# Kernel tuning notes

Hardware: AMD Instinct MI355X
Metric: run time of the kernel (lower is better)

Reference implementation:

```python
import jax, jax.numpy as jnp
import numpy as np

P = 16  # patch size
D = 768  # embedding dim


def setup_inputs() -> dict:
    key = jax.random.key(0)
    k_img, k_w, k_b = jax.random.split(key, 3)
    B, H, W, C = 64, 224, 224, 3
    image = jax.random.normal(k_img, (B, H, W, C), dtype=jnp.float32)
    patch_dim = P * P * C  # 768
    # Keras Dense default: glorot_uniform kernel, zeros bias
    limit = np.sqrt(6.0 / (patch_dim + D)).astype(np.float32)
    W_proj = jax.random.uniform(k_w, (patch_dim, D), dtype=jnp.float32,
                                minval=-limit, maxval=limit)
    b_proj = jnp.zeros((D,), dtype=jnp.float32)
    return {"image": image, "W_proj": W_proj, "b_proj": b_proj}


def reference(image, W_proj, b_proj):
    B, H, W, C = image.shape
    nh, nw = H // P, W // P
    # Fused im2col replacing the per-patch slicing loop:
    # [B,H,W,C] -> [B, nh, P, nw, P, C] -> [B, nh, nw, P, P, C] -> [B, nh*nw, P*P*C]
    # Row-major (p_i, p_j) patch order matches the original nested loop, and
    # flatten of a [B,P,P,C] slice matches the (P,P,C) raveling here.
    patches = image.reshape(B, nh, P, nw, P, C)
    patches = patches.transpose(0, 1, 3, 2, 4, 5).reshape(B, nh * nw, P * P * C)
    # Dense + exact GELU (tf.keras.activations.gelu default approximate=False)
    x = jnp.einsum('bnp,pd->bnd', patches, W_proj) + b_proj
    return jax.nn.gelu(x, approximate=False)
```

## Files before the change

### kernel.cpp

```cpp
#include <hip/hip_runtime.h>
#include <hip/hip_bf16.h>
#include <math.h>

#define MM 12544
#define KK 768
#define NN 768
#define BM 64
#define BN 256
#define BK 64
#define KT 12
#define MT 196
#define NT 3
#define TILE_A_BYTES (BM*BK*2)
#define TILE_B_BYTES (BN*BK*2)

#define IM2COL_BLOCKS ((MM * 96) / 256)
#define WTPACK_BLOCKS ((NN * 96) / 256)

typedef __bf16 v8bf __attribute__((ext_vector_type(8)));
typedef float  v4f  __attribute__((ext_vector_type(4)));

__global__ __launch_bounds__(256) void pack_kernel(const float* __restrict__ img,
                                                   const float* __restrict__ w,
                                                   __hip_bfloat16* __restrict__ apack,
                                                   __hip_bfloat16* __restrict__ wpack) {
    if (blockIdx.x < IM2COL_BLOCKS) {
        int tid = blockIdx.x * 256 + threadIdx.x;
        int gg  = tid % 96;
        int m   = tid / 96;
        int b   = m / 196;
        int pm  = m - b * 196;
        int pr  = pm / 14;
        int pc  = pm - pr * 14;
        int k0  = gg * 8;
        int i   = k0 / 48;
        int rem = k0 - i * 48;
        const float* src = img + (size_t)(((b * 224 + pr * 16 + i) * 224 + pc * 16) * 3 + rem);
        float4 f0 = *(const float4*)src;
        float4 f1 = *(const float4*)(src + 4);
        int mt = m >> 6;
        int r  = m & 63;
        int kt = gg >> 3;
        int g  = gg & 7;
        int gs = g ^ (r & 7);
        union { __hip_bfloat16 h[8]; uint4 u; } o;
        o.h[0] = __float2bfloat16(f0.x); o.h[1] = __float2bfloat16(f0.y);
        o.h[2] = __float2bfloat16(f0.z); o.h[3] = __float2bfloat16(f0.w);
        o.h[4] = __float2bfloat16(f1.x); o.h[5] = __float2bfloat16(f1.y);
        o.h[6] = __float2bfloat16(f1.z); o.h[7] = __float2bfloat16(f1.w);
        *(uint4*)(apack + ((size_t)(mt * KT + kt) * BM + r) * BK + gs * 8) = o.u;
    } else {
        int tid = (blockIdx.x - IM2COL_BLOCKS) * 256 + threadIdx.x;
        int n   = tid % 768;
        int gg  = tid / 768;
        int k0  = gg * 8;
        float f[8];
#pragma unroll
        for (int j = 0; j < 8; j++) f[j] = w[(size_t)(k0 + j) * NN + n];
        int nt = n >> 8;
        int nr = n & 255;
        int kt = gg >> 3;
        int g  = gg & 7;
        int gs = g ^ (nr & 7);
        union { __hip_bfloat16 h[8]; uint4 u; } o;
#pragma unroll
        for (int j = 0; j < 8; j++) o.h[j] = __float2bfloat16(f[j]);
        *(uint4*)(wpack + ((size_t)(nt * KT + kt) * BN + nr) * BK + gs * 8) = o.u;
    }
}

__device__ __forceinline__ float gelu_fast(float x) {
    float t2 = 1.5957691216057308f * x * (1.0f + 0.044715f * x * x);
    float e  = __expf(t2);
    float r  = __builtin_amdgcn_rcpf(e + 1.0f);
    return x - x * r;
}

__global__ __launch_bounds__(256, 3) void gemm_gelu(const __hip_bfloat16* __restrict__ apack,
                                                    const __hip_bfloat16* __restrict__ wpack,
                                                    const float* __restrict__ bias,
                                                    float* __restrict__ out) {
    __shared__ __align__(16) __hip_bfloat16 As[BM * BK];
    __shared__ __align__(16) __hip_bfloat16 Bs[BN * BK];

    const int blk = blockIdx.x;
    const int nt  = blk % 3;
    const int mt  = blk / 3;

    const int tid  = threadIdx.x;
    const int lane = tid & 63;
    const int wave = tid >> 6;
    const int wn   = wave * 64;
    const int col  = lane & 15;
    const int quad = lane >> 4;
    const int cl7  = col & 7;

    v4f acc[4][4];
    const v4f vzero = {0.f, 0.f, 0.f, 0.f};
#pragma unroll
    for (int a = 0; a < 4; a++)
#pragma unroll
        for (int c = 0; c < 4; c++) acc[a][c] = vzero;

    const char* aT = (const char*)apack + (size_t)mt * KT * TILE_A_BYTES;
    const char* bT = (const char*)wpack + (size_t)nt * KT * TILE_B_BYTES;

    for (int kt = 0; kt < KT; kt++) {
#pragma unroll
        for (int p = 0; p < 2; p++) {
            int off = p * 4096 + tid * 16;
            __builtin_amdgcn_global_load_lds(
                (const __attribute__((address_space(1))) void*)(aT + off),
                (__attribute__((address_space(3))) void*)((char*)As + off), 16, 0, 0);
        }
#pragma unroll
        for (int p = 0; p < 8; p++) {
            int off = p * 4096 + tid * 16;
            __builtin_amdgcn_global_load_lds(
                (const __attribute__((address_space(1))) void*)(bT + off),
                (__attribute__((address_space(3))) void*)((char*)Bs + off), 16, 0, 0);
        }
        aT += TILE_A_BYTES;
        bT += TILE_B_BYTES;
        __syncthreads();

#pragma unroll
        for (int ks = 0; ks < 2; ks++) {
            const int gs = (ks * 4 + quad) ^ cl7;
            const v8bf* pa = (const v8bf*)(As + col * BK + gs * 8);
            const v8bf* pb = (const v8bf*)(Bs + (wn + col) * BK + gs * 8);
            v8bf af[4], bfr[4];
#pragma unroll
            for (int mi = 0; mi < 4; mi++) af[mi] = pa[mi * 128];
#pragma unroll
            for (int ni = 0; ni < 4; ni++) bfr[ni] = pb[ni * 128];
#pragma unroll
            for (int mi = 0; mi < 4; mi++)
#pragma unroll
                for (int ni = 0; ni < 4; ni++)
                    acc[mi][ni] = __builtin_amdgcn_mfma_f32_16x16x32_bf16(
                        af[mi], bfr[ni], acc[mi][ni], 0, 0, 0);
        }
        __syncthreads();
    }

#pragma unroll
    for (int ni = 0; ni < 4; ni++) {
        int n    = nt * BN + wn + ni * 16 + col;
        float bv = bias[n];
#pragma unroll
        for (int mi = 0; mi < 4; mi++) {
            int rowb = mt * BM + mi * 16 + quad * 4;
            float* po = out + (size_t)rowb * NN + n;
#pragma unroll
            for (int rg = 0; rg < 4; rg++) {
                float x = acc[mi][ni][rg] + bv;
                po[(size_t)rg * NN] = gelu_fast(x);
            }
        }
    }
}

extern "C" void kernel_launch(void* const* d_in, const int* in_sizes, int n_in,
                              void* d_out, int out_size, void* d_ws, size_t ws_size,
                              hipStream_t stream) {
    const float* img   = (const float*)d_in[0];
    const float* wproj = (const float*)d_in[1];
    const float* bias  = (const float*)d_in[2];
    float* out = (float*)d_out;

    __hip_bfloat16* apack = (__hip_bfloat16*)d_ws;
    __hip_bfloat16* wpack = (__hip_bfloat16*)((char*)d_ws + (size_t)MM * KK * 2);

    pack_kernel<<<dim3(IM2COL_BLOCKS + WTPACK_BLOCKS), dim3(256), 0, stream>>>(
        img, wproj, apack, wpack);
    gemm_gelu<<<dim3(MT * NT), dim3(256), 0, stream>>>(apack, wpack, bias, out);
}
```

Baseline: 118.5 us.

## Fuse im2col and bf16 conversion of image into GEMM A-tile loading

Drops the separate im2col pack pass that wrote a bf16 copy of the patch matrix to workspace. The GEMM now reads fp32 image pixels straight from global memory, converts them to bf16 in registers and stores them into the swizzled LDS A tile. It prefetches the next K-slice into registers one step ahead. This removes the write and re-read of a 19 MB intermediate, but each of the 3 N-tile blocks now re-reads the fp32 image (twice the bytes of bf16) and spends ALU time converting inside the GEMM loop.

New measurement: 123.4 us. 4.1% more time.

```diff
diff --git a/kernel.cpp b/kernel.cpp
--- a/kernel.cpp
+++ b/kernel.cpp
@@ -11,62 +11,31 @@
 #define KT 12
 #define MT 196
 #define NT 3
-#define TILE_A_BYTES (BM*BK*2)
 #define TILE_B_BYTES (BN*BK*2)
 
-#define IM2COL_BLOCKS ((MM * 96) / 256)
 #define WTPACK_BLOCKS ((NN * 96) / 256)
 
 typedef __bf16 v8bf __attribute__((ext_vector_type(8)));
 typedef float  v4f  __attribute__((ext_vector_type(4)));
 
-__global__ __launch_bounds__(256) void pack_kernel(const float* __restrict__ img,
-                                                   const float* __restrict__ w,
-                                                   __hip_bfloat16* __restrict__ apack,
-                                                   __hip_bfloat16* __restrict__ wpack) {
-    if (blockIdx.x < IM2COL_BLOCKS) {
-        int tid = blockIdx.x * 256 + threadIdx.x;
-        int gg  = tid % 96;
-        int m   = tid / 96;
-        int b   = m / 196;
-        int pm  = m - b * 196;
-        int pr  = pm / 14;
-        int pc  = pm - pr * 14;
-        int k0  = gg * 8;
-        int i   = k0 / 48;
-        int rem = k0 - i * 48;
-        const float* src = img + (size_t)(((b * 224 + pr * 16 + i) * 224 + pc * 16) * 3 + rem);
-        float4 f0 = *(const float4*)src;
-        float4 f1 = *(const float4*)(src + 4);
-        int mt = m >> 6;
-        int r  = m & 63;
-        int kt = gg >> 3;
-        int g  = gg & 7;
-        int gs = g ^ (r & 7);
-        union { __hip_bfloat16 h[8]; uint4 u; } o;
-        o.h[0] = __float2bfloat16(f0.x); o.h[1] = __float2bfloat16(f0.y);
-        o.h[2] = __float2bfloat16(f0.z); o.h[3] = __float2bfloat16(f0.w);
-        o.h[4] = __float2bfloat16(f1.x); o.h[5] = __float2bfloat16(f1.y);
-        o.h[6] = __float2bfloat16(f1.z); o.h[7] = __float2bfloat16(f1.w);
-        *(uint4*)(apack + ((size_t)(mt * KT + kt) * BM + r) * BK + gs * 8) = o.u;
-    } else {
-        int tid = (blockIdx.x - IM2COL_BLOCKS) * 256 + threadIdx.x;
-        int n   = tid % 768;
-        int gg  = tid / 768;
-        int k0  = gg * 8;
-        float f[8];
+__global__ __launch_bounds__(256) void wpack_kernel(const float* __restrict__ w,
+                                                    __hip_bfloat16* __restrict__ wpack) {
+    int tid = blockIdx.x * 256 + threadIdx.x;
+    int n   = tid % 768;
+    int gg  = tid / 768;
+    int k0  = gg * 8;
+    float f[8];
 #pragma unroll
-        for (int j = 0; j < 8; j++) f[j] = w[(size_t)(k0 + j) * NN + n];
-        int nt = n >> 8;
-        int nr = n & 255;
-        int kt = gg >> 3;
-        int g  = gg & 7;
-        int gs = g ^ (nr & 7);
-        union { __hip_bfloat16 h[8]; uint4 u; } o;
+    for (int j = 0; j < 8; j++) f[j] = w[(size_t)(k0 + j) * NN + n];
+    int nt = n >> 8;
+    int nr = n & 255;
+    int kt = gg >> 3;
+    int g  = gg & 7;
+    int gs = g ^ (nr & 7);
+    union { __hip_bfloat16 h[8]; uint4 u; } o;
 #pragma unroll
-        for (int j = 0; j < 8; j++) o.h[j] = __float2bfloat16(f[j]);
-        *(uint4*)(wpack + ((size_t)(nt * KT + kt) * BN + nr) * BK + gs * 8) = o.u;
-    }
+    for (int j = 0; j < 8; j++) o.h[j] = __float2bfloat16(f[j]);
+    *(uint4*)(wpack + ((size_t)(nt * KT + kt) * BN + nr) * BK + gs * 8) = o.u;
 }
 
 __device__ __forceinline__ float gelu_fast(float x) {
@@ -76,10 +45,10 @@
     return x - x * r;
 }
 
-__global__ __launch_bounds__(256, 3) void gemm_gelu(const __hip_bfloat16* __restrict__ apack,
-                                                    const __hip_bfloat16* __restrict__ wpack,
-                                                    const float* __restrict__ bias,
-                                                    float* __restrict__ out) {
+__global__ __launch_bounds__(256, 3) void gemm_fused(const float* __restrict__ img,
+                                                     const __hip_bfloat16* __restrict__ wpack,
+                                                     const float* __restrict__ bias,
+                                                     float* __restrict__ out) {
     __shared__ __align__(16) __hip_bfloat16 As[BM * BK];
     __shared__ __align__(16) __hip_bfloat16 Bs[BN * BK];
 
@@ -95,24 +64,38 @@
     const int quad = lane >> 4;
     const int cl7  = col & 7;
 
+    const int r  = tid >> 2;
+    const int c  = tid & 3;
+    const int m  = mt * BM + r;
+    const int b  = m / 196;
+    const int pm = m - b * 196;
+    const int pr = pm / 14;
+    const int pc = pm - pr * 14;
+    const float* abase = img + (size_t)((b * 224 + pr * 16) * 224 + pc * 16) * 3;
+    int rem = (c == 3) ? 0 : c * 16;
+    const float* asrc = abase + ((c == 3) ? 672 : 0) + rem;
+    const int s0 = (2 * c) ^ (r & 7);
+    uint4* aw0 = (uint4*)(As + r * BK + s0 * 8);
+    uint4* aw1 = (uint4*)(As + r * BK + (s0 ^ 1) * 8);
+
     v4f acc[4][4];
     const v4f vzero = {0.f, 0.f, 0.f, 0.f};
 #pragma unroll
     for (int a = 0; a < 4; a++)
 #pragma unroll
-        for (int c = 0; c < 4; c++) acc[a][c] = vzero;
+        for (int cc = 0; cc < 4; cc++) acc[a][cc] = vzero;
 
-    const char* aT = (const char*)apack + (size_t)mt * KT * TILE_A_BYTES;
     const char* bT = (const char*)wpack + (size_t)nt * KT * TILE_B_BYTES;
 
+    float4 a0, a1, a2, a3;
+    {
+        const float4* ap = (const float4*)asrc;
+        a0 = ap[0]; a1 = ap[1]; a2 = ap[2]; a3 = ap[3];
+        asrc += (rem < 32) ? 688 : 1312;
+        rem   = (rem < 32) ? rem + 16 : 0;
+    }
+
     for (int kt = 0; kt < KT; kt++) {
-#pragma unroll
-        for (int p = 0; p < 2; p++) {
-            int off = p * 4096 + tid * 16;
-            __builtin_amdgcn_global_load_lds(
-                (const __attribute__((address_space(1))) void*)(aT + off),
-                (__attribute__((address_space(3))) void*)((char*)As + off), 16, 0, 0);
-        }
 #pragma unroll
         for (int p = 0; p < 8; p++) {
             int off = p * 4096 + tid * 16;
@@ -120,8 +103,26 @@
                 (const __attribute__((address_space(1))) void*)(bT + off),
                 (__attribute__((address_space(3))) void*)((char*)Bs + off), 16, 0, 0);
         }
-        aT += TILE_A_BYTES;
         bT += TILE_B_BYTES;
+
+        union { __hip_bfloat16 h[8]; uint4 u; } o0, o1;
+        o0.h[0] = __float2bfloat16(a0.x); o0.h[1] = __float2bfloat16(a0.y);
+        o0.h[2] = __float2bfloat16(a0.z); o0.h[3] = __float2bfloat16(a0.w);
+        o0.h[4] = __float2bfloat16(a1.x); o0.h[5] = __float2bfloat16(a1.y);
+        o0.h[6] = __float2bfloat16(a1.z); o0.h[7] = __float2bfloat16(a1.w);
+        o1.h[0] = __float2bfloat16(a2.x); o1.h[1] = __float2bfloat16(a2.y);
+        o1.h[2] = __float2bfloat16(a2.z); o1.h[3] = __float2bfloat16(a2.w);
+        o1.h[4] = __float2bfloat16(a3.x); o1.h[5] = __float2bfloat16(a3.y);
+        o1.h[6] = __float2bfloat16(a3.z); o1.h[7] = __float2bfloat16(a3.w);
+        *aw0 = o0.u;
+        *aw1 = o1.u;
+
+        if (kt + 1 < KT) {
+            const float4* ap = (const float4*)asrc;
+            a0 = ap[0]; a1 = ap[1]; a2 = ap[2]; a3 = ap[3];
+            asrc += (rem < 32) ? 688 : 1312;
+            rem   = (rem < 32) ? rem + 16 : 0;
+        }
         __syncthreads();
 
 #pragma unroll
@@ -169,10 +170,8 @@
     const float* bias  = (const float*)d_in[2];
     float* out = (float*)d_out;
 
-    __hip_bfloat16* apack = (__hip_bfloat16*)d_ws;
-    __hip_bfloat16* wpack = (__hip_bfloat16*)((char*)d_ws + (size_t)MM * KK * 2);
+    __hip_bfloat16* wpack = (__hip_bfloat16*)d_ws;
 
-    pack_kernel<<<dim3(IM2COL_BLOCKS + WTPACK_BLOCKS), dim3(256), 0, stream>>>(
-        img, wproj, apack, wpack);
-    gemm_gelu<<<dim3(MT * NT), dim3(256), 0, stream>>>(apack, wpack, bias, out);
+    wpack_kernel<<<dim3(WTPACK_BLOCKS), dim3(256), 0, stream>>>(wproj, wpack);
+    gemm_fused<<<dim3(MT * NT), dim3(256), 0, stream>>>(img, wpack, bias, out);
 }
```

## Pack operands in MFMA fragment order and load fragments directly into registers

Applied to the files above, without the earlier changes.

The pack kernel now writes A and W in per-lane MFMA fragment order, so the GEMM kernel can load its operands straight from global memory into registers. This removes the LDS staging and both __syncthreads per K step, using register double-buffering to prefetch the next K slice instead. Block indices are also remapped so that neighbouring tiles land on the same XCD for L2 reuse. In exchange, A tiles are no longer shared through LDS: each of the four waves loads the same A fragments from global memory, which raises L2 traffic and register pressure.

Measured after the change: 119.8 us. About the same (+1.0%).

```diff
diff --git a/kernel.cpp b/kernel.cpp
--- a/kernel.cpp
+++ b/kernel.cpp
@@ -7,15 +7,16 @@
 #define NN 768
 #define BM 64
 #define BN 256
-#define BK 64
-#define KT 12
+#define NKS 24
 #define MT 196
 #define NT 3
-#define TILE_A_BYTES (BM*BK*2)
-#define TILE_B_BYTES (BN*BK*2)
+#define N64 12
 
-#define IM2COL_BLOCKS ((MM * 96) / 256)
-#define WTPACK_BLOCKS ((NN * 96) / 256)
+#define A_BLOCKS (MT * NKS)
+#define W_BLOCKS (N64 * NKS)
+#define FRAG_BYTES 1024
+#define KSTRIDE (4 * FRAG_BYTES)
+#define PANEL_BYTES (NKS * KSTRIDE)
 
 typedef __bf16 v8bf __attribute__((ext_vector_type(8)));
 typedef float  v4f  __attribute__((ext_vector_type(4)));
@@ -24,48 +25,46 @@
                                                    const float* __restrict__ w,
                                                    __hip_bfloat16* __restrict__ apack,
                                                    __hip_bfloat16* __restrict__ wpack) {
-    if (blockIdx.x < IM2COL_BLOCKS) {
-        int tid = blockIdx.x * 256 + threadIdx.x;
-        int gg  = tid % 96;
-        int m   = tid / 96;
-        int b   = m / 196;
-        int pm  = m - b * 196;
-        int pr  = pm / 14;
-        int pc  = pm - pr * 14;
-        int k0  = gg * 8;
-        int i   = k0 / 48;
-        int rem = k0 - i * 48;
+    const int tid  = threadIdx.x;
+    const int l    = tid & 63;
+    const int fi   = tid >> 6;
+    const int l_lo = l & 15;
+    const int l_hi = l >> 4;
+
+    union { __hip_bfloat16 h[8]; uint4 u; } o;
+
+    if (blockIdx.x < A_BLOCKS) {
+        const int bid = blockIdx.x;
+        const int mt  = bid / NKS;
+        const int ks  = bid - mt * NKS;
+        const int m   = mt * 64 + fi * 16 + l_lo;
+        const int k0  = ks * 32 + l_hi * 8;
+        const int b   = m / 196;
+        const int pm  = m - b * 196;
+        const int pr  = pm / 14;
+        const int pc  = pm - pr * 14;
+        const int i   = k0 / 48;
+        const int rem = k0 - i * 48;
         const float* src = img + (size_t)(((b * 224 + pr * 16 + i) * 224 + pc * 16) * 3 + rem);
         float4 f0 = *(const float4*)src;
         float4 f1 = *(const float4*)(src + 4);
-        int mt = m >> 6;
-        int r  = m & 63;
-        int kt = gg >> 3;
-        int g  = gg & 7;
-        int gs = g ^ (r & 7);
-        union { __hip_bfloat16 h[8]; uint4 u; } o;
         o.h[0] = __float2bfloat16(f0.x); o.h[1] = __float2bfloat16(f0.y);
         o.h[2] = __float2bfloat16(f0.z); o.h[3] = __float2bfloat16(f0.w);
         o.h[4] = __float2bfloat16(f1.x); o.h[5] = __float2bfloat16(f1.y);
         o.h[6] = __float2bfloat16(f1.z); o.h[7] = __float2bfloat16(f1.w);
-        *(uint4*)(apack + ((size_t)(mt * KT + kt) * BM + r) * BK + gs * 8) = o.u;
+        ((uint4*)apack)[(size_t)((mt * NKS + ks) * 4 + fi) * 64 + l] = o.u;
     } else {
-        int tid = (blockIdx.x - IM2COL_BLOCKS) * 256 + threadIdx.x;
-        int n   = tid % 768;
-        int gg  = tid / 768;
-        int k0  = gg * 8;
+        const int bid = blockIdx.x - A_BLOCKS;
+        const int n64 = bid / NKS;
+        const int ks  = bid - n64 * NKS;
+        const int col = n64 * 64 + fi * 16 + l_lo;
+        const int k0  = ks * 32 + l_hi * 8;
         float f[8];
 #pragma unroll
-        for (int j = 0; j < 8; j++) f[j] = w[(size_t)(k0 + j) * NN + n];
-        int nt = n >> 8;
-        int nr = n & 255;
-        int kt = gg >> 3;
-        int g  = gg & 7;
-        int gs = g ^ (nr & 7);
-        union { __hip_bfloat16 h[8]; uint4 u; } o;
+        for (int j = 0; j < 8; j++) f[j] = w[(size_t)(k0 + j) * NN + col];
 #pragma unroll
         for (int j = 0; j < 8; j++) o.h[j] = __float2bfloat16(f[j]);
-        *(uint4*)(wpack + ((size_t)(nt * KT + kt) * BN + nr) * BK + gs * 8) = o.u;
+        ((uint4*)wpack)[(size_t)((n64 * NKS + ks) * 4 + fi) * 64 + l] = o.u;
     }
 }
 
@@ -76,24 +75,25 @@
     return x - x * r;
 }
 
-__global__ __launch_bounds__(256, 3) void gemm_gelu(const __hip_bfloat16* __restrict__ apack,
-                                                    const __hip_bfloat16* __restrict__ wpack,
-                                                    const float* __restrict__ bias,
-                                                    float* __restrict__ out) {
-    __shared__ __align__(16) __hip_bfloat16 As[BM * BK];
-    __shared__ __align__(16) __hip_bfloat16 Bs[BN * BK];
-
-    const int blk = blockIdx.x;
-    const int nt  = blk % 3;
-    const int mt  = blk / 3;
+__global__ __launch_bounds__(256, 3) void gemm_reg(const __hip_bfloat16* __restrict__ apack,
+                                                   const __hip_bfloat16* __restrict__ wpack,
+                                                   const float* __restrict__ bias,
+                                                   float* __restrict__ out) {
+    const int h   = blockIdx.x;
+    const int xcd = h & 7;
+    const int jj  = h >> 3;
+    const int u   = (xcd < 4 ? xcd * 74 : 296 + (xcd - 4) * 73) + jj;
+    const int nt  = u % 3;
+    const int mt  = u / 3;
 
     const int tid  = threadIdx.x;
     const int lane = tid & 63;
     const int wave = tid >> 6;
-    const int wn   = wave * 64;
     const int col  = lane & 15;
     const int quad = lane >> 4;
-    const int cl7  = col & 7;
+
+    const char* pA = (const char*)apack + (size_t)mt * PANEL_BYTES + lane * 16;
+    const char* pB = (const char*)wpack + (size_t)(nt * 4 + wave) * PANEL_BYTES + lane * 16;
 
     v4f acc[4][4];
     const v4f vzero = {0.f, 0.f, 0.f, 0.f};
@@ -102,51 +102,36 @@
 #pragma unroll
         for (int c = 0; c < 4; c++) acc[a][c] = vzero;
 
-    const char* aT = (const char*)apack + (size_t)mt * KT * TILE_A_BYTES;
-    const char* bT = (const char*)wpack + (size_t)nt * KT * TILE_B_BYTES;
+    v8bf aR[2][4], bR[2][4];
+#pragma unroll
+    for (int mi = 0; mi < 4; mi++) aR[0][mi] = *(const v8bf*)(pA + mi * FRAG_BYTES);
+#pragma unroll
+    for (int ni = 0; ni < 4; ni++) bR[0][ni] = *(const v8bf*)(pB + ni * FRAG_BYTES);
 
-    for (int kt = 0; kt < KT; kt++) {
 #pragma unroll
-        for (int p = 0; p < 2; p++) {
-            int off = p * 4096 + tid * 16;
-            __builtin_amdgcn_global_load_lds(
-                (const __attribute__((address_space(1))) void*)(aT + off),
-                (__attribute__((address_space(3))) void*)((char*)As + off), 16, 0, 0);
+    for (int ks = 0; ks < NKS; ks++) {
+        const int cur = ks & 1;
+        if (ks + 1 < NKS) {
+            const char* qA = pA + (size_t)(ks + 1) * KSTRIDE;
+            const char* qB = pB + (size_t)(ks + 1) * KSTRIDE;
+#pragma unroll
+            for (int mi = 0; mi < 4; mi++)
+                aR[cur ^ 1][mi] = *(const v8bf*)(qA + mi * FRAG_BYTES);
+#pragma unroll
+            for (int ni = 0; ni < 4; ni++)
+                bR[cur ^ 1][ni] = *(const v8bf*)(qB + ni * FRAG_BYTES);
         }
 #pragma unroll
-        for (int p = 0; p < 8; p++) {
-            int off = p * 4096 + tid * 16;
-            __builtin_amdgcn_global_load_lds(
-                (const __attribute__((address_space(1))) void*)(bT + off),
-                (__attribute__((address_space(3))) void*)((char*)Bs + off), 16, 0, 0);
-        }
-        aT += TILE_A_BYTES;
-        bT += TILE_B_BYTES;
-        __syncthreads();
-
+        for (int mi = 0; mi < 4; mi++)
 #pragma unroll
-        for (int ks = 0; ks < 2; ks++) {
-            const int gs = (ks * 4 + quad) ^ cl7;
-            const v8bf* pa = (const v8bf*)(As + col * BK + gs * 8);
-            const v8bf* pb = (const v8bf*)(Bs + (wn + col) * BK + gs * 8);
-            v8bf af[4], bfr[4];
-#pragma unroll
-            for (int mi = 0; mi < 4; mi++) af[mi] = pa[mi * 128];
-#pragma unroll
-            for (int ni = 0; ni < 4; ni++) bfr[ni] = pb[ni * 128];
-#pragma unroll
-            for (int mi = 0; mi < 4; mi++)
-#pragma unroll
-                for (int ni = 0; ni < 4; ni++)
-                    acc[mi][ni] = __builtin_amdgcn_mfma_f32_16x16x32_bf16(
-                        af[mi], bfr[ni], acc[mi][ni], 0, 0, 0);
-        }
-        __syncthreads();
+            for (int ni = 0; ni < 4; ni++)
+                acc[mi][ni] = __builtin_amdgcn_mfma_f32_16x16x32_bf16(
+                    aR[cur][mi], bR[cur][ni], acc[mi][ni], 0, 0, 0);
     }
 
 #pragma unroll
     for (int ni = 0; ni < 4; ni++) {
-        int n    = nt * BN + wn + ni * 16 + col;
+        int n    = nt * BN + wave * 64 + ni * 16 + col;
         float bv = bias[n];
 #pragma unroll
         for (int mi = 0; mi < 4; mi++) {
@@ -172,7 +157,7 @@
     __hip_bfloat16* apack = (__hip_bfloat16*)d_ws;
     __hip_bfloat16* wpack = (__hip_bfloat16*)((char*)d_ws + (size_t)MM * KK * 2);
 
-    pack_kernel<<<dim3(IM2COL_BLOCKS + WTPACK_BLOCKS), dim3(256), 0, stream>>>(
+    pack_kernel<<<dim3(A_BLOCKS + W_BLOCKS), dim3(256), 0, stream>>>(
         img, wproj, apack, wpack);
-    gemm_gelu<<<dim3(MT * NT), dim3(256), 0, stream>>>(apack, wpack, bias, out);
+    gemm_reg<<<dim3(MT * NT), dim3(256), 0, stream>>>(apack, wpack, bias, out);
 }
```
